# Kernel tuning notes

Hardware: AMD Instinct MI355X
Metric: run time of the kernel (lower is better)

## Reference

```python
import jax, jax.numpy as jnp
import numpy as np

BATCH = 4
N = 50000   # mesh nodes
LAT = 10    # latent dim n
K = 32      # neighbours per node
M = [64, 64, 256]  # hotness MLP dims; M[-1] = number of clusters
MU = 1.0
B0 = 2.0


def _linear_params(key, out_dim, in_dim):
    kw, _ = jax.random.split(key)
    w = jax.random.normal(kw, (out_dim, in_dim), jnp.float32) * np.sqrt(2.0 / in_dim)
    b = jnp.zeros((out_dim,), jnp.float32)
    return w, b


def setup_inputs() -> dict:
    key = jax.random.key(0)
    ks = jax.random.split(key, 12)
    x = jax.random.normal(ks[0], (BATCH, N), jnp.float32)
    neighbour_id = jax.random.randint(ks[1], (N, K), 0, N)
    # small distances so bubble windows have nonzero support everywhere
    neighbour_distance = jax.random.uniform(ks[2], (N, K), jnp.float32) * 0.05
    clustering_labels = jax.random.randint(ks[3], (N,), 0, M[-1])
    enc1_w, enc1_b = _linear_params(ks[4], 200, N)
    enc2_w, enc2_b = _linear_params(ks[5], LAT, 200)
    dec_w, dec_b = _linear_params(ks[6], N, LAT)
    h1_w, h1_b = _linear_params(ks[7], M[0], LAT)
    h2_w, h2_b = _linear_params(ks[8], M[1], M[0])
    h3_w, h3_b = _linear_params(ks[9], M[2], M[1])
    B_param = jnp.array(B0, jnp.float32)
    return dict(x=x, neighbour_id=neighbour_id, neighbour_distance=neighbour_distance,
                clustering_labels=clustering_labels,
                enc1_w=enc1_w, enc1_b=enc1_b, enc2_w=enc2_w, enc2_b=enc2_b,
                dec_w=dec_w, dec_b=dec_b,
                h1_w=h1_w, h1_b=h1_b, h2_w=h2_w, h2_b=h2_b, h3_w=h3_w, h3_b=h3_b,
                B_param=B_param)


def _silu(v):
    return v * jax.nn.sigmoid(v)


def reference(x, neighbour_id, neighbour_distance, clustering_labels,
              enc1_w, enc1_b, enc2_w, enc2_b, dec_w, dec_b,
              h1_w, h1_b, h2_w, h2_b, h3_w, h3_b, B_param):
    # encode: [b, N] -> [b, n]
    z = _silu(x @ enc1_w.T + enc1_b)
    e = z @ enc2_w.T + enc2_b  # [b, n]

    # hotness MLP on latent codes (batched over b): silu on all but last layer
    h = _silu(e @ h1_w.T + h1_b)
    h = _silu(h @ h2_w.T + h2_b)
    h = h @ h3_w.T + h3_b
    h = jax.nn.sigmoid(h * 0.005)  # [b, n_clusters]

    # per-node hotness via cluster labels -> per-sample, per-basis bandwidths
    H = h[:, clustering_labels]  # [b, N]
    exps = jnp.arange(1, LAT + 1, dtype=jnp.float32)  # [n]
    w = (1.0 - H / 2.0)[:, None, :] ** exps[None, :, None] * B_param  # [b, n, N]

    # RBF bubble window over neighbours, normalized over k
    d2 = neighbour_distance ** 2  # [N, k]
    win = jnp.maximum(0.0, 1.0 - d2[None, None, :, :] / (w * MU)[..., None] ** 2)  # [b,n,N,k]
    win = win / jnp.sum(win, axis=-1, keepdims=True)

    # gather decoder basis rows at neighbours: dec_w.T is [n, N]
    basis = dec_w.T[:, neighbour_id]  # [n, N, k]
    conv = jnp.einsum('nNk,bnNk->bnN', basis, win)  # convolved basis [b, n, N]

    out = jnp.einsum('bn,bnN->bN', e, conv) + dec_b  # [b, N]
    return out
```

## Files before the change

kernel.cpp:

```cpp
#include <hip/hip_runtime.h>
#include <math.h>

#define NN        50000
#define BATCH     4
#define LAT       10
#define KNB       32
#define E1OUT     200
#define NCHUNK    8
#define CHUNK     6250
#define CHUNK2    3125

__device__ __forceinline__ float silu_f(float v) {
    return v / (1.0f + expf(-v));
}

__global__ __launch_bounds__(256) void k1_partial(const float* __restrict__ x,
                                                  const float* __restrict__ w,
                                                  float* __restrict__ partials) {
    const int bx  = blockIdx.x;
    const int r   = bx >> 3;
    const int c   = bx & 7;
    const int tid = threadIdx.x;

    const float2* wr = (const float2*)w + (size_t)r * 25000 + c * CHUNK2;
    const float2* x0 = (const float2*)x + 0 * 25000 + c * CHUNK2;
    const float2* x1 = (const float2*)x + 1 * 25000 + c * CHUNK2;
    const float2* x2 = (const float2*)x + 2 * 25000 + c * CHUNK2;
    const float2* x3 = (const float2*)x + 3 * 25000 + c * CHUNK2;

    float a0 = 0.f, a1 = 0.f, a2 = 0.f, a3 = 0.f;
    for (int j = tid; j < CHUNK2; j += 256) {
        float2 wv = wr[j];
        float2 v0 = x0[j], v1 = x1[j], v2 = x2[j], v3 = x3[j];
        a0 = fmaf(wv.x, v0.x, fmaf(wv.y, v0.y, a0));
        a1 = fmaf(wv.x, v1.x, fmaf(wv.y, v1.y, a1));
        a2 = fmaf(wv.x, v2.x, fmaf(wv.y, v2.y, a2));
        a3 = fmaf(wv.x, v3.x, fmaf(wv.y, v3.y, a3));
    }

    __shared__ float sm[4][256];
    sm[0][tid] = a0; sm[1][tid] = a1; sm[2][tid] = a2; sm[3][tid] = a3;
    __syncthreads();
    for (int s = 128; s > 0; s >>= 1) {
        if (tid < s) {
            sm[0][tid] += sm[0][tid + s];
            sm[1][tid] += sm[1][tid + s];
            sm[2][tid] += sm[2][tid + s];
            sm[3][tid] += sm[3][tid + s];
        }
        __syncthreads();
    }
    if (tid < 4) partials[bx * 4 + tid] = sm[tid][0];
}

__global__ __launch_bounds__(256) void k2_small(
        const float* __restrict__ partials,
        const float* __restrict__ enc1_b,
        const float* __restrict__ enc2_w, const float* __restrict__ enc2_b,
        const float* __restrict__ h1_w,   const float* __restrict__ h1_b,
        const float* __restrict__ h2_w,   const float* __restrict__ h2_b,
        const float* __restrict__ h3_w,   const float* __restrict__ h3_b,
        float* __restrict__ ws_e, float* __restrict__ ws_h) {
    __shared__ float zs[BATCH][E1OUT];
    __shared__ float es[BATCH][LAT];
    __shared__ float h1s[BATCH][64];
    __shared__ float h2s[BATCH][64];
    const int t = threadIdx.x;

    if (t < E1OUT) {
        float a0 = 0.f, a1 = 0.f, a2 = 0.f, a3 = 0.f;
        for (int cc = 0; cc < NCHUNK; ++cc) {
            const float* p = partials + (t * NCHUNK + cc) * 4;
            a0 += p[0]; a1 += p[1]; a2 += p[2]; a3 += p[3];
        }
        float bias = enc1_b[t];
        zs[0][t] = silu_f(a0 + bias);
        zs[1][t] = silu_f(a1 + bias);
        zs[2][t] = silu_f(a2 + bias);
        zs[3][t] = silu_f(a3 + bias);
    }
    __syncthreads();

    if (t < BATCH * LAT) {
        int b = t / LAT, l = t % LAT;
        const float* wrow = enc2_w + l * E1OUT;
        float a = 0.f;
        for (int o = 0; o < E1OUT; ++o) a = fmaf(zs[b][o], wrow[o], a);
        a += enc2_b[l];
        es[b][l] = a;
        ws_e[b * LAT + l] = a;
    }
    __syncthreads();

    {
        int b = t >> 6, u = t & 63;
        float a = h1_b[u];
        const float* wrow = h1_w + u * LAT;
        #pragma unroll
        for (int l = 0; l < LAT; ++l) a = fmaf(es[b][l], wrow[l], a);
        h1s[b][u] = silu_f(a);
    }
    __syncthreads();

    {
        int b = t >> 6, u = t & 63;
        float a = h2_b[u];
        const float* wrow = h2_w + u * 64;
        for (int j = 0; j < 64; ++j) a = fmaf(h1s[b][j], wrow[j], a);
        h2s[b][u] = silu_f(a);
    }
    __syncthreads();

    {
        const float* wrow = h3_w + t * 64;
        float bias = h3_b[t];
        #pragma unroll
        for (int b = 0; b < BATCH; ++b) {
            float a = bias;
            for (int j = 0; j < 64; ++j) a = fmaf(h2s[b][j], wrow[j], a);
            ws_h[b * 256 + t] = 1.0f / (1.0f + expf(-0.005f * a));
        }
    }
}

__global__ __launch_bounds__(256) void k3_main(
        const int*   __restrict__ nid,
        const float* __restrict__ nd,
        const int*   __restrict__ labels,
        const float* __restrict__ dec_w,
        const float* __restrict__ dec_b,
        const float* __restrict__ Bp,
        const float* __restrict__ ws_e,
        const float* __restrict__ ws_h,
        float* __restrict__ out) {
    __shared__ float hs[BATCH * 256];
    __shared__ float es[BATCH * LAT];
    const int tid = threadIdx.x;
    for (int i = tid; i < BATCH * 256; i += 256) hs[i] = ws_h[i];
    if (tid < BATCH * LAT) es[tid] = ws_e[tid];
    __syncthreads();

    const int gid = blockIdx.x * 256 + tid;
    const int n   = gid >> 1;
    const int bs  = gid & 1;
    if (n >= NN) return;

    const float Bv = Bp[0];
    const int   c  = labels[n];

    float invw2[2][LAT];
    #pragma unroll
    for (int bb = 0; bb < 2; ++bb) {
        const int b = bs * 2 + bb;
        const float H    = hs[b * 256 + c];
        const float base = 1.0f - 0.5f * H;
        float cur = base;
        #pragma unroll
        for (int l = 0; l < LAT; ++l) {
            float wv = cur * Bv;
            invw2[bb][l] = 1.0f / (wv * wv);
            cur *= base;
        }
    }

    float num[2][LAT], den[2][LAT];
    #pragma unroll
    for (int bb = 0; bb < 2; ++bb)
        #pragma unroll
        for (int l = 0; l < LAT; ++l) { num[bb][l] = 0.f; den[bb][l] = 0.f; }

    const int4*   nid4 = (const int4*)(nid + (size_t)n * KNB);
    const float4* nd4  = (const float4*)(nd  + (size_t)n * KNB);
    const float2* dw2  = (const float2*)dec_w;

    #pragma unroll
    for (int kk = 0; kk < KNB / 4; ++kk) {
        const int4   id4 = nid4[kk];
        const float4 dd4 = nd4[kk];
        const int   ids[4] = {id4.x, id4.y, id4.z, id4.w};
        const float dsv[4] = {dd4.x, dd4.y, dd4.z, dd4.w};
        #pragma unroll
        for (int q = 0; q < 4; ++q) {
            const float d2 = dsv[q] * dsv[q];
            const float2* brow = dw2 + (size_t)ids[q] * 5;
            const float2 b01 = brow[0], b23 = brow[1], b45 = brow[2],
                         b67 = brow[3], b89 = brow[4];
            const float bas[LAT] = {b01.x, b01.y, b23.x, b23.y, b45.x,
                                    b45.y, b67.x, b67.y, b89.x, b89.y};
            #pragma unroll
            for (int bb = 0; bb < 2; ++bb) {
                #pragma unroll
                for (int l = 0; l < LAT; ++l) {
                    float t = fmaf(-d2, invw2[bb][l], 1.0f);
                    t = fmaxf(t, 0.0f);
                    den[bb][l] += t;
                    num[bb][l]  = fmaf(t, bas[l], num[bb][l]);
                }
            }
        }
    }

    const float dbv = dec_b[n];
    #pragma unroll
    for (int bb = 0; bb < 2; ++bb) {
        const int b = bs * 2 + bb;
        float acc = 0.f;
        #pragma unroll
        for (int l = 0; l < LAT; ++l)
            acc += es[b * LAT + l] * (num[bb][l] / den[bb][l]);
        out[(size_t)b * NN + n] = acc + dbv;
    }
}

extern "C" void kernel_launch(void* const* d_in, const int* in_sizes, int n_in,
                              void* d_out, int out_size, void* d_ws, size_t ws_size,
                              hipStream_t stream) {
    const float* x      = (const float*)d_in[0];
    const int*   nid    = (const int*)  d_in[1];
    const float* nd     = (const float*)d_in[2];
    const int*   labels = (const int*)  d_in[3];
    const float* enc1_w = (const float*)d_in[4];
    const float* enc1_b = (const float*)d_in[5];
    const float* enc2_w = (const float*)d_in[6];
    const float* enc2_b = (const float*)d_in[7];
    const float* dec_w  = (const float*)d_in[8];
    const float* dec_b  = (const float*)d_in[9];
    const float* h1_w   = (const float*)d_in[10];
    const float* h1_b   = (const float*)d_in[11];
    const float* h2_w   = (const float*)d_in[12];
    const float* h2_b   = (const float*)d_in[13];
    const float* h3_w   = (const float*)d_in[14];
    const float* h3_b   = (const float*)d_in[15];
    const float* Bp     = (const float*)d_in[16];

    float* ws       = (float*)d_ws;
    float* partials = ws;
    float* ws_e     = ws + 6400;
    float* ws_h     = ws + 6440;
    float* out      = (float*)d_out;

    k1_partial<<<E1OUT * NCHUNK, 256, 0, stream>>>(x, enc1_w, partials);
    k2_small<<<1, 256, 0, stream>>>(partials, enc1_b, enc2_w, enc2_b,
                                    h1_w, h1_b, h2_w, h2_b, h3_w, h3_b,
                                    ws_e, ws_h);
    const int k3_threads = NN * 2;
    k3_main<<<(k3_threads + 255) / 256, 256, 0, stream>>>(
        nid, nd, labels, dec_w, dec_b, Bp, ws_e, ws_h, out);
}
```

Baseline: 170.7 us.

## Split k3 work across 8 threads per node and pad decoder rows to 16

The main kernel now gives each node 8 threads, one per batch sample and neighbour half, where before it used 2 threads each handling two samples. The halves are combined with a warp shuffle. A new pre-kernel copies dec_w into a 16-float padded layout in the workspace so each gathered row loads with aligned float4/float2 reads. This is meant to raise occupancy and parallelism and cut per-thread register pressure. In exchange it adds a 3.2 MB copy kernel on every call, and each thread now redundantly loads neighbour ids and gathers decoder rows that other threads of the same node also load.

New measurement: 179.1 us. +4.9%, slower.

```diff
diff --git a/kernel.cpp b/kernel.cpp
--- a/kernel.cpp
+++ b/kernel.cpp
@@ -7,11 +7,18 @@
 #define KNB       32
 #define E1OUT     200
 #define NCHUNK    8
-#define CHUNK     6250
 #define CHUNK2    3125
 
 __device__ __forceinline__ float silu_f(float v) {
     return v / (1.0f + expf(-v));
+}
+
+__global__ __launch_bounds__(256) void k0_pad(const float* __restrict__ dec_w,
+                                              float* __restrict__ dec_pad) {
+    const int i = blockIdx.x * 256 + threadIdx.x;
+    if (i >= NN * 16) return;
+    const int r = i >> 4, c = i & 15;
+    dec_pad[i] = (c < LAT) ? dec_w[r * LAT + c] : 0.0f;
 }
 
 __global__ __launch_bounds__(256) void k1_partial(const float* __restrict__ x,
@@ -127,7 +134,7 @@
         const int*   __restrict__ nid,
         const float* __restrict__ nd,
         const int*   __restrict__ labels,
-        const float* __restrict__ dec_w,
+        const float* __restrict__ dec_pad,
         const float* __restrict__ dec_b,
         const float* __restrict__ Bp,
         const float* __restrict__ ws_e,
@@ -141,40 +148,36 @@
     __syncthreads();
 
     const int gid = blockIdx.x * 256 + tid;
-    const int n   = gid >> 1;
-    const int bs  = gid & 1;
+    const int n   = gid >> 3;
     if (n >= NN) return;
+    const int b   = tid & 3;
+    const int kh  = (tid >> 2) & 1;
 
     const float Bv = Bp[0];
     const int   c  = labels[n];
 
-    float invw2[2][LAT];
-    #pragma unroll
-    for (int bb = 0; bb < 2; ++bb) {
-        const int b = bs * 2 + bb;
+    float invw2[LAT];
+    {
         const float H    = hs[b * 256 + c];
         const float base = 1.0f - 0.5f * H;
         float cur = base;
         #pragma unroll
         for (int l = 0; l < LAT; ++l) {
-            float wv = cur * Bv;
-            invw2[bb][l] = 1.0f / (wv * wv);
+            const float wv = cur * Bv;
+            invw2[l] = 1.0f / (wv * wv);
             cur *= base;
         }
     }
 
-    float num[2][LAT], den[2][LAT];
+    float num[LAT], den[LAT];
     #pragma unroll
-    for (int bb = 0; bb < 2; ++bb)
-        #pragma unroll
-        for (int l = 0; l < LAT; ++l) { num[bb][l] = 0.f; den[bb][l] = 0.f; }
-
-    const int4*   nid4 = (const int4*)(nid + (size_t)n * KNB);
-    const float4* nd4  = (const float4*)(nd  + (size_t)n * KNB);
-    const float2* dw2  = (const float2*)dec_w;
+    for (int l = 0; l < LAT; ++l) { num[l] = 0.f; den[l] = 0.f; }
+
+    const int4*   nid4 = (const int4*)nid + (size_t)n * 8 + kh * 4;
+    const float4* nd4  = (const float4*)nd  + (size_t)n * 8 + kh * 4;
 
     #pragma unroll
-    for (int kk = 0; kk < KNB / 4; ++kk) {
+    for (int kk = 0; kk < 4; ++kk) {
         const int4   id4 = nid4[kk];
         const float4 dd4 = nd4[kk];
         const int   ids[4] = {id4.x, id4.y, id4.z, id4.w};
@@ -182,33 +185,35 @@
         #pragma unroll
         for (int q = 0; q < 4; ++q) {
             const float d2 = dsv[q] * dsv[q];
-            const float2* brow = dw2 + (size_t)ids[q] * 5;
-            const float2 b01 = brow[0], b23 = brow[1], b45 = brow[2],
-                         b67 = brow[3], b89 = brow[4];
-            const float bas[LAT] = {b01.x, b01.y, b23.x, b23.y, b45.x,
-                                    b45.y, b67.x, b67.y, b89.x, b89.y};
+            const float* row = dec_pad + (size_t)ids[q] * 16;
+            const float4 r0 = *(const float4*)(row);
+            const float4 r1 = *(const float4*)(row + 4);
+            const float2 r2 = *(const float2*)(row + 8);
+            const float bas[LAT] = {r0.x, r0.y, r0.z, r0.w,
+                                    r1.x, r1.y, r1.z, r1.w,
+                                    r2.x, r2.y};
             #pragma unroll
-            for (int bb = 0; bb < 2; ++bb) {
-                #pragma unroll
-                for (int l = 0; l < LAT; ++l) {
-                    float t = fmaf(-d2, invw2[bb][l], 1.0f);
-                    t = fmaxf(t, 0.0f);
-                    den[bb][l] += t;
-                    num[bb][l]  = fmaf(t, bas[l], num[bb][l]);
-                }
+            for (int l = 0; l < LAT; ++l) {
+                float t = fmaf(-d2, invw2[l], 1.0f);
+                t = fmaxf(t, 0.0f);
+                den[l] += t;
+                num[l]  = fmaf(t, bas[l], num[l]);
             }
         }
     }
 
-    const float dbv = dec_b[n];
     #pragma unroll
-    for (int bb = 0; bb < 2; ++bb) {
-        const int b = bs * 2 + bb;
+    for (int l = 0; l < LAT; ++l) {
+        num[l] += __shfl_xor(num[l], 4);
+        den[l] += __shfl_xor(den[l], 4);
+    }
+
+    if (kh == 0) {
         float acc = 0.f;
         #pragma unroll
         for (int l = 0; l < LAT; ++l)
-            acc += es[b * LAT + l] * (num[bb][l] / den[bb][l]);
-        out[(size_t)b * NN + n] = acc + dbv;
+            acc = fmaf(es[b * LAT + l], num[l] / den[l], acc);
+        out[(size_t)b * NN + n] = acc + dec_b[n];
     }
 }
 
@@ -237,13 +242,15 @@
     float* partials = ws;
     float* ws_e     = ws + 6400;
     float* ws_h     = ws + 6440;
+    float* dec_pad  = ws + 8192;
     float* out      = (float*)d_out;
 
+    k0_pad<<<(NN * 16 + 255) / 256, 256, 0, stream>>>(dec_w, dec_pad);
     k1_partial<<<E1OUT * NCHUNK, 256, 0, stream>>>(x, enc1_w, partials);
     k2_small<<<1, 256, 0, stream>>>(partials, enc1_b, enc2_w, enc2_b,
                                     h1_w, h1_b, h2_w, h2_b, h3_w, h3_b,
                                     ws_e, ws_h);
-    const int k3_threads = NN * 2;
+    const int k3_threads = NN * 8;
     k3_main<<<(k3_threads + 255) / 256, 256, 0, stream>>>(
-        nid, nd, labels, dec_w, dec_b, Bp, ws_e, ws_h, out);
-}
+        nid, nd, labels, dec_pad, dec_b, Bp, ws_e, ws_h, out);
+}
```
